# Kernel tuning notes

Hardware: AMD Instinct MI355X
Metric: run time of the kernel (lower is better)

## Reference

```python
import jax, jax.numpy as jnp
import numpy as np

N = 50000
E = 800000
D = 128
O = 128


def _spmm_coo(rows, cols, vals, x, n_rows):
    # out[r] += vals[e] * x[cols[e]]  (COO sparse matrix times dense matrix)
    gathered = vals[:, None] * x[cols]            # [E, O]
    return jax.ops.segment_sum(gathered, rows, num_segments=n_rows)


def setup_inputs() -> dict:
    key = jax.random.key(0)
    ks = jax.random.split(key, 9)
    return {
        "inputs": jax.random.normal(ks[0], (N, D), dtype=jnp.float32),
        "adj1_rows": jax.random.randint(ks[1], (E,), 0, N, dtype=jnp.int32),
        "adj1_cols": jax.random.randint(ks[2], (E,), 0, N, dtype=jnp.int32),
        "adj1_vals": jax.random.uniform(ks[3], (E,), dtype=jnp.float32),
        "adj2_rows": jax.random.randint(ks[4], (E,), 0, N, dtype=jnp.int32),
        "adj2_cols": jax.random.randint(ks[5], (E,), 0, N, dtype=jnp.int32),
        "adj2_vals": jax.random.uniform(ks[6], (E,), dtype=jnp.float32),
        "weights_1": jax.random.normal(ks[7], (D, O), dtype=jnp.float32) * (6.0 / (D + O)) ** 0.5,
        "weights_2": jax.random.normal(ks[8], (D, O), dtype=jnp.float32) * (6.0 / (D + O)) ** 0.5,
    }


def reference(inputs, adj1_rows, adj1_cols, adj1_vals,
              adj2_rows, adj2_cols, adj2_vals, weights_1, weights_2):
    # dense projection per relation
    x1 = inputs @ weights_1                        # [N, O]
    x2 = inputs @ weights_2                        # [N, O]
    # sparse aggregation per relation
    y1 = _spmm_coo(adj1_rows, adj1_cols, adj1_vals, x1, N)
    y2 = _spmm_coo(adj2_rows, adj2_cols, adj2_vals, x2, N)
    return jax.nn.relu(y1 + y2)
```

## Files before the change

### kernel.cpp

```cpp
#include <hip/hip_runtime.h>


typedef __attribute__((ext_vector_type(4))) float     f32x4;
typedef __attribute__((ext_vector_type(8))) short     bf16x8;

#define NB      782
#define BSLOTS  10
#define BCAP    2560
#define SCAP    64

static __device__ __forceinline__ unsigned short f2bf(float f) {
    unsigned u = __float_as_uint(f);
    u += 0x7FFF + ((u >> 16) & 1);
    return (unsigned short)(u >> 16);
}

__global__ __launch_bounds__(256) void convert_kernel(
    const float* __restrict__ X,
    const float* __restrict__ W1, const float* __restrict__ W2,
    unsigned short* __restrict__ Xb, unsigned short* __restrict__ Wt, int n)
{
    const int stride = gridDim.x * blockDim.x;
    const int nW = 2 * 128 * 128;
    const int nX = n * 32;
    const int total = nW + nX;
    for (int g = blockIdx.x * blockDim.x + threadIdx.x; g < total; g += stride) {
        if (g < nW) {
            const int rel = g >> 14;
            const int o   = (g >> 7) & 127;
            const int k   = g & 127;
            const float* W = rel ? W2 : W1;
            Wt[g] = f2bf(W[k * 128 + o]);
        } else {
            const int i = g - nW;
            const float4 v = ((const float4*)X)[i];
            ushort4 b;
            b.x = f2bf(v.x); b.y = f2bf(v.y); b.z = f2bf(v.z); b.w = f2bf(v.w);
            ((ushort4*)Xb)[i] = b;
        }
    }
}

__global__ __launch_bounds__(256) void bin_kernel(
    const int* __restrict__ rows1, const int* __restrict__ cols1, const float* __restrict__ vals1,
    const int* __restrict__ rows2, const int* __restrict__ cols2, const float* __restrict__ vals2,
    int* __restrict__ gcur, unsigned long long* __restrict__ edges_tmp,
    int E, int n)
{
    __shared__ unsigned long long stage[NB][BSLOTS];
    __shared__ int scnt[NB];

    for (int i = threadIdx.x; i < NB; i += 256) scnt[i] = 0;
    __syncthreads();

    const int stride = gridDim.x * 256;
    const int total  = 2 * E;
    for (int g = blockIdx.x * 256 + threadIdx.x; g < total; g += stride) {
        int r, col, rel; float v;
        if (g < E) { r = rows1[g]; col = cols1[g]; rel = 0; v = vals1[g]; }
        else       { int e = g - E; r = rows2[e]; col = cols2[e]; rel = 1; v = vals2[e]; }

        const int b = r >> 6;
        const unsigned lo = (unsigned)(r & 63) | ((unsigned)rel << 6) | ((unsigned)col << 7);
        const unsigned long long pack =
            (unsigned long long)lo | ((unsigned long long)__float_as_uint(v) << 32);

        const int pos = atomicAdd(&scnt[b], 1);
        if (pos < BSLOTS) {
            stage[b][pos] = pack;
        } else {
            int gp = atomicAdd(&gcur[b], 1);
            if (gp < BCAP) edges_tmp[(size_t)b * BCAP + gp] = pack;
        }
    }
    __syncthreads();

    for (int b = threadIdx.x; b < NB; b += 256) {
        int k = scnt[b]; if (k > BSLOTS) k = BSLOTS;
        if (k > 0) {
            int base = atomicAdd(&gcur[b], k);
            for (int i = 0; i < k; ++i)
                if (base + i < BCAP)
                    edges_tmp[(size_t)b * BCAP + base + i] = stage[b][i];
        }
    }
}

__global__ __launch_bounds__(256) void agg_kernel(
    const int* __restrict__ gcur,
    const unsigned long long* __restrict__ edges_tmp,
    const unsigned short* __restrict__ Xb,
    unsigned short* __restrict__ agg, int n)
{
    __shared__ unsigned long long lists[32 * SCAP];
    __shared__ int cnt[32];

    const int nwg = NB * 4;
    const int xcd = blockIdx.x & 7, bi = blockIdx.x >> 3;
    const int q8 = nwg >> 3;
    const int swz = xcd * q8 + bi;

    const int b   = swz >> 2;
    const int q   = swz & 3;
    const int tid = threadIdx.x;
    const int rowbase = b * 64 + q * 16;
    if (rowbase >= n) return;

    int sz = gcur[b]; if (sz > BCAP) sz = BCAP;
    const unsigned long long* ebase = edges_tmp + (size_t)b * BCAP;

    if (tid < 32) cnt[tid] = 0;
    __syncthreads();

    for (int e = tid; e < sz; e += 256) {
        const unsigned long long p = ebase[e];
        const unsigned lo = (unsigned)p;
        const int rl = (int)(lo & 63u);
        if ((rl >> 4) == q) {
            const int seg = ((rl & 15) << 1) | ((lo >> 6) & 1);
            const int pos = atomicAdd(&cnt[seg], 1);
            if (pos < SCAP) lists[seg * SCAP + pos] = p;
        }
    }
    __syncthreads();

    const int lane = tid & 31;
    const int grp  = tid >> 5;
    for (int seg = grp; seg < 32; seg += 8) {
        const int row = rowbase + (seg >> 1);
        if (row >= n) continue;
        const int rel = seg & 1;
        int m = cnt[seg]; if (m > SCAP) m = SCAP;
        const unsigned long long* lst = &lists[seg * SCAP];
        float4 acc = make_float4(0.f, 0.f, 0.f, 0.f);

        int e = 0;
        for (; e + 4 <= m; e += 4) {
            const unsigned long long p0 = lst[e + 0];
            const unsigned long long p1 = lst[e + 1];
            const unsigned long long p2 = lst[e + 2];
            const unsigned long long p3 = lst[e + 3];
            const ushort4 x0 = *(const ushort4*)&Xb[(size_t)(((unsigned)p0 >> 7) & 0xFFFFu) * 128 + lane * 4];
            const ushort4 x1 = *(const ushort4*)&Xb[(size_t)(((unsigned)p1 >> 7) & 0xFFFFu) * 128 + lane * 4];
            const ushort4 x2 = *(const ushort4*)&Xb[(size_t)(((unsigned)p2 >> 7) & 0xFFFFu) * 128 + lane * 4];
            const ushort4 x3 = *(const ushort4*)&Xb[(size_t)(((unsigned)p3 >> 7) & 0xFFFFu) * 128 + lane * 4];
            const float v0 = __uint_as_float((unsigned)(p0 >> 32));
            const float v1 = __uint_as_float((unsigned)(p1 >> 32));
            const float v2 = __uint_as_float((unsigned)(p2 >> 32));
            const float v3 = __uint_as_float((unsigned)(p3 >> 32));
            acc.x = fmaf(v0, __uint_as_float((unsigned)x0.x << 16), acc.x);
            acc.y = fmaf(v0, __uint_as_float((unsigned)x0.y << 16), acc.y);
            acc.z = fmaf(v0, __uint_as_float((unsigned)x0.z << 16), acc.z);
            acc.w = fmaf(v0, __uint_as_float((unsigned)x0.w << 16), acc.w);
            acc.x = fmaf(v1, __uint_as_float((unsigned)x1.x << 16), acc.x);
            acc.y = fmaf(v1, __uint_as_float((unsigned)x1.y << 16), acc.y);
            acc.z = fmaf(v1, __uint_as_float((unsigned)x1.z << 16), acc.z);
            acc.w = fmaf(v1, __uint_as_float((unsigned)x1.w << 16), acc.w);
            acc.x = fmaf(v2, __uint_as_float((unsigned)x2.x << 16), acc.x);
            acc.y = fmaf(v2, __uint_as_float((unsigned)x2.y << 16), acc.y);
            acc.z = fmaf(v2, __uint_as_float((unsigned)x2.z << 16), acc.z);
            acc.w = fmaf(v2, __uint_as_float((unsigned)x2.w << 16), acc.w);
            acc.x = fmaf(v3, __uint_as_float((unsigned)x3.x << 16), acc.x);
            acc.y = fmaf(v3, __uint_as_float((unsigned)x3.y << 16), acc.y);
            acc.z = fmaf(v3, __uint_as_float((unsigned)x3.z << 16), acc.z);
            acc.w = fmaf(v3, __uint_as_float((unsigned)x3.w << 16), acc.w);
        }
        for (; e < m; ++e) {
            const unsigned long long p = lst[e];
            const ushort4 xv = *(const ushort4*)&Xb[(size_t)(((unsigned)p >> 7) & 0xFFFFu) * 128 + lane * 4];
            const float v  = __uint_as_float((unsigned)(p >> 32));
            acc.x = fmaf(v, __uint_as_float((unsigned)xv.x << 16), acc.x);
            acc.y = fmaf(v, __uint_as_float((unsigned)xv.y << 16), acc.y);
            acc.z = fmaf(v, __uint_as_float((unsigned)xv.z << 16), acc.z);
            acc.w = fmaf(v, __uint_as_float((unsigned)xv.w << 16), acc.w);
        }

        ushort4 o;
        o.x = f2bf(acc.x); o.y = f2bf(acc.y); o.z = f2bf(acc.z); o.w = f2bf(acc.w);
        *(ushort4*)&agg[((size_t)rel * n + row) * 128 + lane * 4] = o;
    }
}

__global__ __launch_bounds__(256) void gemm_relu_kernel(
    const unsigned short* __restrict__ agg,
    const unsigned short* __restrict__ Wt,
    float* __restrict__ out, int n)
{
    const int lane = threadIdx.x & 63;
    const int w    = threadIdx.x >> 6;
    const int colbase = w * 32;
    const int l15 = lane & 15;
    const int lhi = lane >> 4;

    bf16x8 bfrag[2][2][4];
    #pragma unroll
    for (int rel = 0; rel < 2; ++rel) {
        const unsigned short* Wr = Wt + rel * 16384;
        #pragma unroll
        for (int ct = 0; ct < 2; ++ct) {
            const int o = colbase + ct * 16 + l15;
            #pragma unroll
            for (int ks = 0; ks < 4; ++ks)
                bfrag[rel][ct][ks] = *(const bf16x8*)&Wr[o * 128 + ks * 32 + lhi * 8];
        }
    }

    const int row0 = blockIdx.x * 32;
    const f32x4 zero = {0.f, 0.f, 0.f, 0.f};

    #pragma unroll
    for (int rt = 0; rt < 2; ++rt) {
        const int r0 = row0 + rt * 16;
        int ra = r0 + l15; if (ra >= n) ra = n - 1;
        bf16x8 af0[4], af1[4];
        #pragma unroll
        for (int ks = 0; ks < 4; ++ks) {
            af0[ks] = *(const bf16x8*)&agg[(size_t)ra * 128 + ks * 32 + lhi * 8];
            af1[ks] = *(const bf16x8*)&agg[((size_t)n + ra) * 128 + ks * 32 + lhi * 8];
        }

        f32x4 acc[2];
        acc[0] = zero; acc[1] = zero;
        #pragma unroll
        for (int ks = 0; ks < 4; ++ks) {
            acc[0] = __builtin_amdgcn_mfma_f32_16x16x32_bf16(af0[ks], bfrag[0][0][ks], acc[0], 0, 0, 0);
            acc[1] = __builtin_amdgcn_mfma_f32_16x16x32_bf16(af0[ks], bfrag[0][1][ks], acc[1], 0, 0, 0);
            acc[0] = __builtin_amdgcn_mfma_f32_16x16x32_bf16(af1[ks], bfrag[1][0][ks], acc[0], 0, 0, 0);
            acc[1] = __builtin_amdgcn_mfma_f32_16x16x32_bf16(af1[ks], bfrag[1][1][ks], acc[1], 0, 0, 0);
        }

        #pragma unroll
        for (int ct = 0; ct < 2; ++ct) {
            const int col = colbase + ct * 16 + l15;
            #pragma unroll
            for (int j = 0; j < 4; ++j) {
                const int r = r0 + lhi * 4 + j;
                if (r < n) out[(size_t)r * 128 + col] = fmaxf(acc[ct][j], 0.f);
            }
        }
    }
}

extern "C" void kernel_launch(void* const* d_in, const int* in_sizes, int n_in,
                              void* d_out, int out_size, void* d_ws, size_t ws_size,
                              hipStream_t stream)
{
    const float* X  = (const float*)d_in[0];
    const int*   r1 = (const int*)  d_in[1];
    const int*   c1 = (const int*)  d_in[2];
    const float* v1 = (const float*)d_in[3];
    const int*   r2 = (const int*)  d_in[4];
    const int*   c2 = (const int*)  d_in[5];
    const float* v2 = (const float*)d_in[6];
    const float* W1 = (const float*)d_in[7];
    const float* W2 = (const float*)d_in[8];
    float*       out = (float*)d_out;

    const int n = in_sizes[0] / 128;
    const int E = in_sizes[1];

    unsigned short* agg = (unsigned short*)d_ws;
    unsigned short* Xb  = agg + (size_t)2 * n * 128;
    unsigned short* Wt  = Xb + (size_t)n * 128;
    unsigned long long* edges_tmp =
        (unsigned long long*)(((uintptr_t)(Wt + 2 * 128 * 128) + 255) & ~(uintptr_t)255);
    int* gcur = (int*)(edges_tmp + (size_t)NB * BCAP);

    hipMemsetAsync(gcur, 0, NB * sizeof(int), stream);

    convert_kernel<<<2048, 256, 0, stream>>>(X, W1, W2, Xb, Wt, n);

    bin_kernel<<<512, 256, 0, stream>>>(r1, c1, v1, r2, c2, v2, gcur, edges_tmp, E, n);

    agg_kernel<<<NB * 4, 256, 0, stream>>>(gcur, edges_tmp, Xb, agg, n);

    gemm_relu_kernel<<<(n + 31) / 32, 256, 0, stream>>>(agg, Wt, out, n);
}
```

Measured before the change: 129.8 us.

## Fuse convert with binning and aggregation with GEMM-ReLU kernels

```diff
diff --git a/kernel.cpp b/kernel.cpp
--- a/kernel.cpp
+++ b/kernel.cpp
@@ -8,52 +8,58 @@
 #define BSLOTS  10
 #define BCAP    2560
 #define SCAP    64
+#define BING    512
+#define CONVG   256
+#define TPITCH  136
 
 static __device__ __forceinline__ unsigned short f2bf(float f) {
     unsigned u = __float_as_uint(f);
     u += 0x7FFF + ((u >> 16) & 1);
     return (unsigned short)(u >> 16);
 }
-
-__global__ __launch_bounds__(256) void convert_kernel(
+static __device__ __forceinline__ float b2f(unsigned short s) {
+    return __uint_as_float((unsigned)s << 16);
+}
+
+__global__ __launch_bounds__(256) void convbin_kernel(
     const float* __restrict__ X,
     const float* __restrict__ W1, const float* __restrict__ W2,
-    unsigned short* __restrict__ Xb, unsigned short* __restrict__ Wt, int n)
-{
-    const int stride = gridDim.x * blockDim.x;
-    const int nW = 2 * 128 * 128;
-    const int nX = n * 32;
-    const int total = nW + nX;
-    for (int g = blockIdx.x * blockDim.x + threadIdx.x; g < total; g += stride) {
-        if (g < nW) {
-            const int rel = g >> 14;
-            const int o   = (g >> 7) & 127;
-            const int k   = g & 127;
-            const float* W = rel ? W2 : W1;
-            Wt[g] = f2bf(W[k * 128 + o]);
-        } else {
-            const int i = g - nW;
-            const float4 v = ((const float4*)X)[i];
-            ushort4 b;
-            b.x = f2bf(v.x); b.y = f2bf(v.y); b.z = f2bf(v.z); b.w = f2bf(v.w);
-            ((ushort4*)Xb)[i] = b;
-        }
-    }
-}
-
-__global__ __launch_bounds__(256) void bin_kernel(
     const int* __restrict__ rows1, const int* __restrict__ cols1, const float* __restrict__ vals1,
     const int* __restrict__ rows2, const int* __restrict__ cols2, const float* __restrict__ vals2,
+    unsigned short* __restrict__ Xb, unsigned short* __restrict__ Wt,
     int* __restrict__ gcur, unsigned long long* __restrict__ edges_tmp,
     int E, int n)
 {
+    if (blockIdx.x >= BING) {
+        const int stride = CONVG * 256;
+        const int nW = 2 * 128 * 128;
+        const int nX = n * 32;
+        const int total = nW + nX;
+        for (int g = (blockIdx.x - BING) * 256 + threadIdx.x; g < total; g += stride) {
+            if (g < nW) {
+                const int rel = g >> 14;
+                const int o   = (g >> 7) & 127;
+                const int k   = g & 127;
+                const float* W = rel ? W2 : W1;
+                Wt[g] = f2bf(W[k * 128 + o]);
+            } else {
+                const int i = g - nW;
+                const float4 v = ((const float4*)X)[i];
+                ushort4 b;
+                b.x = f2bf(v.x); b.y = f2bf(v.y); b.z = f2bf(v.z); b.w = f2bf(v.w);
+                ((ushort4*)Xb)[i] = b;
+            }
+        }
+        return;
+    }
+
     __shared__ unsigned long long stage[NB][BSLOTS];
     __shared__ int scnt[NB];
 
     for (int i = threadIdx.x; i < NB; i += 256) scnt[i] = 0;
     __syncthreads();
 
-    const int stride = gridDim.x * 256;
+    const int stride = BING * 256;
     const int total  = 2 * E;
     for (int g = blockIdx.x * 256 + threadIdx.x; g < total; g += stride) {
         int r, col, rel; float v;
@@ -86,25 +92,45 @@
     }
 }
 
-__global__ __launch_bounds__(256) void agg_kernel(
+__global__ __launch_bounds__(256) void aggemm_kernel(
     const int* __restrict__ gcur,
     const unsigned long long* __restrict__ edges_tmp,
     const unsigned short* __restrict__ Xb,
-    unsigned short* __restrict__ agg, int n)
+    const unsigned short* __restrict__ Wt,
+    float* __restrict__ out, int n)
 {
     __shared__ unsigned long long lists[32 * SCAP];
     __shared__ int cnt[32];
-
-    const int nwg = NB * 4;
+    __shared__ unsigned short tile[2 * 16 * TPITCH];
+
+    const int tid = threadIdx.x;
+    const int NQ  = NB * 4;
     const int xcd = blockIdx.x & 7, bi = blockIdx.x >> 3;
-    const int q8 = nwg >> 3;
-    const int swz = xcd * q8 + bi;
+    const int swz = xcd * (NQ >> 3) + bi;
 
     const int b   = swz >> 2;
     const int q   = swz & 3;
-    const int tid = threadIdx.x;
-    const int rowbase = b * 64 + q * 16;
+    const int rowbase = swz * 16;
     if (rowbase >= n) return;
+
+    const int lane64 = tid & 63;
+    const int w      = tid >> 6;
+    const int colbase = w * 32;
+    const int l15 = lane64 & 15;
+    const int lhi = lane64 >> 4;
+
+    bf16x8 bfrag[2][2][4];
+    #pragma unroll
+    for (int rel = 0; rel < 2; ++rel) {
+        const unsigned short* Wr = Wt + rel * 16384;
+        #pragma unroll
+        for (int ct = 0; ct < 2; ++ct) {
+            const int o = colbase + ct * 16 + l15;
+            #pragma unroll
+            for (int ks = 0; ks < 4; ++ks)
+                bfrag[rel][ct][ks] = *(const bf16x8*)&Wr[o * 128 + ks * 32 + lhi * 8];
+        }
+    }
 
     int sz = gcur[b]; if (sz > BCAP) sz = BCAP;
     const unsigned long long* ebase = edges_tmp + (size_t)b * BCAP;
@@ -148,95 +174,64 @@
             const float v1 = __uint_as_float((unsigned)(p1 >> 32));
             const float v2 = __uint_as_float((unsigned)(p2 >> 32));
             const float v3 = __uint_as_float((unsigned)(p3 >> 32));
-            acc.x = fmaf(v0, __uint_as_float((unsigned)x0.x << 16), acc.x);
-            acc.y = fmaf(v0, __uint_as_float((unsigned)x0.y << 16), acc.y);
-            acc.z = fmaf(v0, __uint_as_float((unsigned)x0.z << 16), acc.z);
-            acc.w = fmaf(v0, __uint_as_float((unsigned)x0.w << 16), acc.w);
-            acc.x = fmaf(v1, __uint_as_float((unsigned)x1.x << 16), acc.x);
-            acc.y = fmaf(v1, __uint_as_float((unsigned)x1.y << 16), acc.y);
-            acc.z = fmaf(v1, __uint_as_float((unsigned)x1.z << 16), acc.z);
-            acc.w = fmaf(v1, __uint_as_float((unsigned)x1.w << 16), acc.w);
-            acc.x = fmaf(v2, __uint_as_float((unsigned)x2.x << 16), acc.x);
-            acc.y = fmaf(v2, __uint_as_float((unsigned)x2.y << 16), acc.y);
-            acc.z = fmaf(v2, __uint_as_float((unsigned)x2.z << 16), acc.z);
-            acc.w = fmaf(v2, __uint_as_float((unsigned)x2.w << 16), acc.w);
-            acc.x = fmaf(v3, __uint_as_float((unsigned)x3.x << 16), acc.x);
-            acc.y = fmaf(v3, __uint_as_float((unsigned)x3.y << 16), acc.y);
-            acc.z = fmaf(v3, __uint_as_float((unsigned)x3.z << 16), acc.z);
-            acc.w = fmaf(v3, __uint_as_float((unsigned)x3.w << 16), acc.w);
+            acc.x = fmaf(v0, b2f(x0.x), acc.x);
+            acc.y = fmaf(v0, b2f(x0.y), acc.y);
+            acc.z = fmaf(v0, b2f(x0.z), acc.z);
+            acc.w = fmaf(v0, b2f(x0.w), acc.w);
+            acc.x = fmaf(v1, b2f(x1.x), acc.x);
+            acc.y = fmaf(v1, b2f(x1.y), acc.y);
+            acc.z = fmaf(v1, b2f(x1.z), acc.z);
+            acc.w = fmaf(v1, b2f(x1.w), acc.w);
+            acc.x = fmaf(v2, b2f(x2.x), acc.x);
+            acc.y = fmaf(v2, b2f(x2.y), acc.y);
+            acc.z = fmaf(v2, b2f(x2.z), acc.z);
+            acc.w = fmaf(v2, b2f(x2.w), acc.w);
+            acc.x = fmaf(v3, b2f(x3.x), acc.x);
+            acc.y = fmaf(v3, b2f(x3.y), acc.y);
+            acc.z = fmaf(v3, b2f(x3.z), acc.z);
+            acc.w = fmaf(v3, b2f(x3.w), acc.w);
         }
         for (; e < m; ++e) {
             const unsigned long long p = lst[e];
             const ushort4 xv = *(const ushort4*)&Xb[(size_t)(((unsigned)p >> 7) & 0xFFFFu) * 128 + lane * 4];
             const float v  = __uint_as_float((unsigned)(p >> 32));
-            acc.x = fmaf(v, __uint_as_float((unsigned)xv.x << 16), acc.x);
-            acc.y = fmaf(v, __uint_as_float((unsigned)xv.y << 16), acc.y);
-            acc.z = fmaf(v, __uint_as_float((unsigned)xv.z << 16), acc.z);
-            acc.w = fmaf(v, __uint_as_float((unsigned)xv.w << 16), acc.w);
+            acc.x = fmaf(v, b2f(xv.x), acc.x);
+            acc.y = fmaf(v, b2f(xv.y), acc.y);
+            acc.z = fmaf(v, b2f(xv.z), acc.z);
+            acc.w = fmaf(v, b2f(xv.w), acc.w);
         }
 
         ushort4 o;
         o.x = f2bf(acc.x); o.y = f2bf(acc.y); o.z = f2bf(acc.z); o.w = f2bf(acc.w);
-        *(ushort4*)&agg[((size_t)rel * n + row) * 128 + lane * 4] = o;
-    }
-}
-
-__global__ __launch_bounds__(256) void gemm_relu_kernel(
-    const unsigned short* __restrict__ agg,
-    const unsigned short* __restrict__ Wt,
-    float* __restrict__ out, int n)
-{
-    const int lane = threadIdx.x & 63;
-    const int w    = threadIdx.x >> 6;
-    const int colbase = w * 32;
-    const int l15 = lane & 15;
-    const int lhi = lane >> 4;
-
-    bf16x8 bfrag[2][2][4];
-    #pragma unroll
-    for (int rel = 0; rel < 2; ++rel) {
-        const unsigned short* Wr = Wt + rel * 16384;
+        *(ushort4*)&tile[(rel * 16 + (seg >> 1)) * TPITCH + lane * 4] = o;
+    }
+    __syncthreads();
+
+    bf16x8 af0[4], af1[4];
+    #pragma unroll
+    for (int ks = 0; ks < 4; ++ks) {
+        af0[ks] = *(const bf16x8*)&tile[(0 * 16 + l15) * TPITCH + ks * 32 + lhi * 8];
+        af1[ks] = *(const bf16x8*)&tile[(1 * 16 + l15) * TPITCH + ks * 32 + lhi * 8];
+    }
+
+    const f32x4 zero = {0.f, 0.f, 0.f, 0.f};
+    f32x4 acc[2];
+    acc[0] = zero; acc[1] = zero;
+    #pragma unroll
+    for (int ks = 0; ks < 4; ++ks) {
+        acc[0] = __builtin_amdgcn_mfma_f32_16x16x32_bf16(af0[ks], bfrag[0][0][ks], acc[0], 0, 0, 0);
+        acc[1] = __builtin_amdgcn_mfma_f32_16x16x32_bf16(af0[ks], bfrag[0][1][ks], acc[1], 0, 0, 0);
+        acc[0] = __builtin_amdgcn_mfma_f32_16x16x32_bf16(af1[ks], bfrag[1][0][ks], acc[0], 0, 0, 0);
+        acc[1] = __builtin_amdgcn_mfma_f32_16x16x32_bf16(af1[ks], bfrag[1][1][ks], acc[1], 0, 0, 0);
+    }
+
+    #pragma unroll
+    for (int ct = 0; ct < 2; ++ct) {
+        const int col = colbase + ct * 16 + l15;
         #pragma unroll
-        for (int ct = 0; ct < 2; ++ct) {
-            const int o = colbase + ct * 16 + l15;
-            #pragma unroll
-            for (int ks = 0; ks < 4; ++ks)
-                bfrag[rel][ct][ks] = *(const bf16x8*)&Wr[o * 128 + ks * 32 + lhi * 8];
-        }
-    }
-
-    const int row0 = blockIdx.x * 32;
-    const f32x4 zero = {0.f, 0.f, 0.f, 0.f};
-
-    #pragma unroll
-    for (int rt = 0; rt < 2; ++rt) {
-        const int r0 = row0 + rt * 16;
-        int ra = r0 + l15; if (ra >= n) ra = n - 1;
-        bf16x8 af0[4], af1[4];
-        #pragma unroll
-        for (int ks = 0; ks < 4; ++ks) {
-            af0[ks] = *(const bf16x8*)&agg[(size_t)ra * 128 + ks * 32 + lhi * 8];
-            af1[ks] = *(const bf16x8*)&agg[((size_t)n + ra) * 128 + ks * 32 + lhi * 8];
-        }
-
-        f32x4 acc[2];
-        acc[0] = zero; acc[1] = zero;
-        #pragma unroll
-        for (int ks = 0; ks < 4; ++ks) {
-            acc[0] = __builtin_amdgcn_mfma_f32_16x16x32_bf16(af0[ks], bfrag[0][0][ks], acc[0], 0, 0, 0);
-            acc[1] = __builtin_amdgcn_mfma_f32_16x16x32_bf16(af0[ks], bfrag[0][1][ks], acc[1], 0, 0, 0);
-            acc[0] = __builtin_amdgcn_mfma_f32_16x16x32_bf16(af1[ks], bfrag[1][0][ks], acc[0], 0, 0, 0);
-            acc[1] = __builtin_amdgcn_mfma_f32_16x16x32_bf16(af1[ks], bfrag[1][1][ks], acc[1], 0, 0, 0);
-        }
-
-        #pragma unroll
-        for (int ct = 0; ct < 2; ++ct) {
-            const int col = colbase + ct * 16 + l15;
-            #pragma unroll
-            for (int j = 0; j < 4; ++j) {
-                const int r = r0 + lhi * 4 + j;
-                if (r < n) out[(size_t)r * 128 + col] = fmaxf(acc[ct][j], 0.f);
-            }
+        for (int j = 0; j < 4; ++j) {
+            const int r = rowbase + lhi * 4 + j;
+            if (r < n) out[(size_t)r * 128 + col] = fmaxf(acc[ct][j], 0.f);
         }
     }
 }
@@ -259,20 +254,16 @@
     const int n = in_sizes[0] / 128;
     const int E = in_sizes[1];
 
-    unsigned short* agg = (unsigned short*)d_ws;
-    unsigned short* Xb  = agg + (size_t)2 * n * 128;
-    unsigned short* Wt  = Xb + (size_t)n * 128;
+    unsigned short* Xb = (unsigned short*)d_ws;
+    unsigned short* Wt = Xb + (size_t)n * 128;
     unsigned long long* edges_tmp =
         (unsigned long long*)(((uintptr_t)(Wt + 2 * 128 * 128) + 255) & ~(uintptr_t)255);
     int* gcur = (int*)(edges_tmp + (size_t)NB * BCAP);
 
     hipMemsetAsync(gcur, 0, NB * sizeof(int), stream);
 
-    convert_kernel<<<2048, 256, 0, stream>>>(X, W1, W2, Xb, Wt, n);
-
-    bin_kernel<<<512, 256, 0, stream>>>(r1, c1, v1, r2, c2, v2, gcur, edges_tmp, E, n);
-
-    agg_kernel<<<NB * 4, 256, 0, stream>>>(gcur, edges_tmp, Xb, agg, n);
-
-    gemm_relu_kernel<<<(n + 31) / 32, 256, 0, stream>>>(agg, Wt, out, n);
-}
+    convbin_kernel<<<BING + CONVG, 256, 0, stream>>>(
+        X, W1, W2, r1, c1, v1, r2, c2, v2, Xb, Wt, gcur, edges_tmp, E, n);
+
+    aggemm_kernel<<<NB * 4, 256, 0, stream>>>(gcur, edges_tmp, Xb, Wt, out, n);
+}
```

Result: slower. 137.6 us (median of 2 runs) (+6.0%).
